# Kernel tuning notes

Measured on AMD Instinct MI355X. Metric: run time of the kernel, lower is better.

The kernel has to match this reference:

```python
import jax, jax.numpy as jnp
import numpy as np
from jax import lax

C = 64
KD = 16  # in_channels // k_factor
KS = 3
DN = ('NCHW', 'OIHW', 'NCHW')


def setup_inputs() -> dict:
    key = jax.random.key(0)
    ks = jax.random.split(key, 9)
    B, H, W = 4, 128, 128
    s = 0.05
    return {
        'x': jax.random.normal(ks[0], (B, C, H, W), jnp.float32),
        'y': jax.random.normal(ks[1], (B, C, H, W), jnp.float32),
        'z': jax.random.normal(ks[2], (B, C, H, W), jnp.float32),
        'Wq': jax.random.normal(ks[3], (C, 1, KS, KS), jnp.float32) * s,   # depthwise
        'bq': jax.random.normal(ks[4], (C,), jnp.float32) * s,
        'Wk': jax.random.normal(ks[5], (KD, C, KS, KS), jnp.float32) * s,
        'bk': jax.random.normal(ks[6], (KD,), jnp.float32) * s,
        'wv': jax.random.normal(ks[7], (KD,), jnp.float32) * s,           # 1x1 conv 1->KD
        'bv': jax.random.normal(ks[8], (KD,), jnp.float32) * s,
    }


def reference(x, y, z, Wq, bq, Wk, bk, wv, bv):
    # Q: depthwise 3x3 conv + ReLU on y -> [B,C,H,W]
    q = jax.nn.relu(
        lax.conv_general_dilated(y, Wq, (1, 1), 'SAME',
                                 dimension_numbers=DN, feature_group_count=C)
        + bq[None, :, None, None])
    # K: 3x3 conv C->KD + ReLU on x -> [B,KD,H,W], shared across the C channel axis
    k = jax.nn.relu(
        lax.conv_general_dilated(x, Wk, (1, 1), 'SAME', dimension_numbers=DN)
        + bk[None, :, None, None])
    # V: 1x1 conv 1->KD + ReLU applied per input channel of z -> [B,C,KD,H,W]
    v = jax.nn.relu(z[:, :, None] * wv[None, None, :, None, None]
                    + bv[None, None, :, None, None])
    # Degenerate SDPA: head_dim=1 so scale=1; softmax over the KD 'sequence' axis.
    scores = q[:, :, None] * k[:, None]              # [B,C,KD,H,W]
    attn = jax.nn.softmax(scores, axis=2)
    return jnp.sum(attn * v, axis=2)                 # [B,C,H,W]
```

## Files before the change

kernel.cpp:

```cpp
#include <hip/hip_runtime.h>

#define HH 128
#define WW 128
#define CC 64
#define KD 16
#define HW (HH * WW)
#define HWB (HW * 4)
#define TOTBYTES (4u * CC * HW * 4u)
#define OOB_SENT 0x40000000

using int32x4_t = __attribute__((ext_vector_type(4))) int;
using floatx4   = __attribute__((ext_vector_type(4))) float;

__device__ floatx4 llvm_amdgcn_raw_buffer_load_v4f32(int32x4_t srsrc, int voffset,
                                                     int soffset, int aux)
    __asm("llvm.amdgcn.raw.buffer.load.v4f32");
__device__ float llvm_amdgcn_raw_buffer_load_f32(int32x4_t srsrc, int voffset,
                                                 int soffset, int aux)
    __asm("llvm.amdgcn.raw.buffer.load.f32");

__device__ inline int32x4_t make_srd(const void* p, unsigned bytes) {
    const unsigned long long a = (unsigned long long)p;
    int32x4_t r;
    r.x = (int)(a & 0xffffffffull);
    r.y = (int)(a >> 32);
    r.z = (int)bytes;
    r.w = 0x00020000;
    return r;
}

#if __has_builtin(__builtin_amdgcn_exp2f)
#define FAST_EXP2(x) __builtin_amdgcn_exp2f(x)
#define KLOG2E 1.44269504088896340736f
#else
#define FAST_EXP2(x) __expf(x)
#define KLOG2E 1.0f
#endif

__global__ __launch_bounds__(512, 8) void gatev_fused(
    const float* __restrict__ x, const float* __restrict__ y,
    const float* __restrict__ z,
    const float* __restrict__ Wq, const float* __restrict__ bq,
    const float* __restrict__ Wk, const float* __restrict__ bk,
    const float* __restrict__ wv, const float* __restrict__ bv,
    float* __restrict__ out)
{
    __shared__ float part[8 * KD * 64];

    const int tid  = threadIdx.x;
    const int g    = __builtin_amdgcn_readfirstlane(tid >> 6);
    const int lane = tid & 63;
    const int px   = lane & 15, py = lane >> 4;
    const int b    = blockIdx.z;
    const int h    = blockIdx.y * 4 + py;
    const int w    = blockIdx.x * 16 + px;
    const int pix  = h * WW + w;

    const int32x4_t rx = make_srd(x, TOTBYTES);
    const int32x4_t ry = make_srd(y, TOTBYTES);
    const int32x4_t rz = make_srd(z, TOTBYTES);

    const int colb = (w > 0 ? w - 1 : 0) * 4;
    int rowB[3];
#pragma unroll
    for (int r = 0; r < 3; ++r) {
        const int rr = h - 1 + r;
        rowB[r] = (rr >= 0 && rr < HH) ? rr * WW * 4 + colb : OOB_SENT;
    }
    const float mL = (w > 0) ? 1.f : 0.f;
    const float mR = (w < WW - 1) ? 1.f : 0.f;
    const bool  w0 = (w == 0);

    const int base = b * CC * HWB;
    const int c0   = __builtin_amdgcn_readfirstlane(g * 8);

    auto taps9 = [&](const int32x4_t& srd, int so, float (&tp)[9]) {
#pragma unroll
        for (int r = 0; r < 3; ++r) {
            const floatx4 f = llvm_amdgcn_raw_buffer_load_v4f32(srd, rowB[r], so, 0);
            tp[r * 3 + 0] = f.x * mL;
            tp[r * 3 + 1] = w0 ? f.x : f.y;
            tp[r * 3 + 2] = (w0 ? f.y : f.z) * mR;
        }
    };

    float acc[KD];
#pragma unroll
    for (int d = 0; d < KD; ++d) acc[d] = 0.f;

    for (int ci = 0; ci < 8; ++ci) {
        const int c = c0 + ci;
        float tp[9];
        taps9(rx, base + c * HWB, tp);
        const float* wp = Wk + c * 9;
#pragma unroll
        for (int d = 0; d < KD; ++d)
#pragma unroll
            for (int t = 0; t < 9; ++t)
                acc[d] = fmaf(wp[d * (CC * 9) + t], tp[t], acc[d]);
    }
#pragma unroll
    for (int d = 0; d < KD; ++d)
        part[g * (KD * 64) + d * 64 + lane] = acc[d];
    __syncthreads();

#pragma unroll
    for (int rep = 0; rep < 2; ++rep) {
        const int idx = tid + rep * 512;
        float s = part[idx];
#pragma unroll
        for (int gg = 1; gg < 8; ++gg) s += part[gg * (KD * 64) + idx];
        const int d = idx >> 6;
        part[idx] = fmaxf(s + bk[d], 0.f) * KLOG2E;
    }
    __syncthreads();

    float q[8], zv[8];
#pragma unroll 2
    for (int ci = 0; ci < 8; ++ci) {
        const int c  = c0 + ci;
        const int so = base + c * HWB;
        float tp[9];
        taps9(ry, so, tp);
        const float* wq = Wq + c * 9;
        float a = 0.f;
#pragma unroll
        for (int t = 0; t < 9; ++t) a = fmaf(wq[t], tp[t], a);
        q[ci]  = fmaxf(a + bq[c], 0.f);
        zv[ci] = llvm_amdgcn_raw_buffer_load_f32(rz, pix * 4, so, 0);
    }

    float num[8], den[8];
#pragma unroll
    for (int ci = 0; ci < 8; ++ci) { num[ci] = 0.f; den[ci] = 0.f; }

#pragma unroll
    for (int d = 0; d < KD; ++d) {
        const float kl  = part[d * 64 + lane];
        const float wvd = wv[d];
        const float bvd = bv[d];
#pragma unroll
        for (int ci = 0; ci < 8; ++ci) {
            const float e = FAST_EXP2(q[ci] * kl);
            const float v = fmaxf(zv[ci] * wvd + bvd, 0.f);
            num[ci] = fmaf(e, v, num[ci]);
            den[ci] += e;
        }
    }

    float* ob = out + (size_t)b * CC * HW;
#pragma unroll
    for (int ci = 0; ci < 8; ++ci)
        ob[(c0 + ci) * HW + pix] = __fdividef(num[ci], den[ci]);
}

extern "C" void kernel_launch(void* const* d_in, const int* in_sizes, int n_in,
                              void* d_out, int out_size, void* d_ws, size_t ws_size,
                              hipStream_t stream) {
    const float* x  = (const float*)d_in[0];
    const float* y  = (const float*)d_in[1];
    const float* z  = (const float*)d_in[2];
    const float* Wq = (const float*)d_in[3];
    const float* bq = (const float*)d_in[4];
    const float* Wk = (const float*)d_in[5];
    const float* bk = (const float*)d_in[6];
    const float* wv = (const float*)d_in[7];
    const float* bv = (const float*)d_in[8];
    float* out = (float*)d_out;

    dim3 grid(WW / 16, HH / 4, 4);
    dim3 block(512);
    hipLaunchKernelGGL(gatev_fused, grid, block, 0, stream,
                       x, y, z, Wq, bq, Wk, bk, wv, bv, out);
}
```

Before: 51.18 us.

## Compute K convolution with FP16 MFMA from an LDS-staged halo tile

Replaces the per-thread scalar FP32 3x3 C->KD convolution with an implicit GEMM on MFMA 16x16x32 f16 instructions. The x halo tile (6x18x64) and the Wk weights are converted to fp16 and staged in swizzled LDS, and eight waves each cover one output row and one half of the channels. The partial-sum reduction shrinks from 8 groups to 2. This cuts the FP32 FMA work of the K conv, at the cost of fp16 rounding of the inputs and weights (a precision risk), a larger LDS footprint that may lower occupancy, and an extra barrier.

Measured after the change: 84.38 us. 64.9% more time.

```diff
diff --git a/kernel.cpp b/kernel.cpp
--- a/kernel.cpp
+++ b/kernel.cpp
@@ -9,8 +9,9 @@
 #define TOTBYTES (4u * CC * HW * 4u)
 #define OOB_SENT 0x40000000
 
-using int32x4_t = __attribute__((ext_vector_type(4))) int;
-using floatx4   = __attribute__((ext_vector_type(4))) float;
+typedef __attribute__((ext_vector_type(4))) int   int32x4_t;
+typedef __attribute__((ext_vector_type(4))) float floatx4;
+typedef _Float16 f16x8 __attribute__((ext_vector_type(8)));
 
 __device__ floatx4 llvm_amdgcn_raw_buffer_load_v4f32(int32x4_t srsrc, int voffset,
                                                      int soffset, int aux)
@@ -45,88 +46,131 @@
     const float* __restrict__ wv, const float* __restrict__ bv,
     float* __restrict__ out)
 {
-    __shared__ float part[8 * KD * 64];
+    __shared__ __align__(16) unsigned char smem[40960];
+    unsigned short* xt   = (unsigned short*)smem;
+    unsigned short* wkl  = (unsigned short*)(smem + 14336);
+    float*          part = (float*)(smem + 32768);
 
     const int tid  = threadIdx.x;
     const int g    = __builtin_amdgcn_readfirstlane(tid >> 6);
     const int lane = tid & 63;
     const int px   = lane & 15, py = lane >> 4;
     const int b    = blockIdx.z;
-    const int h    = blockIdx.y * 4 + py;
-    const int w    = blockIdx.x * 16 + px;
+    const int h0   = blockIdx.y * 4;
+    const int w0   = blockIdx.x * 16;
+    const int h    = h0 + py;
+    const int w    = w0 + px;
     const int pix  = h * WW + w;
 
     const int32x4_t rx = make_srd(x, TOTBYTES);
     const int32x4_t ry = make_srd(y, TOTBYTES);
     const int32x4_t rz = make_srd(z, TOTBYTES);
 
+    const int base = b * CC * HWB;
+
+#pragma unroll
+    for (int rep = 0; rep < 7; ++rep) {
+        const int idx2 = tid + rep * 512;
+        const int e0   = idx2 * 2;
+        const int c    = e0 & 63;
+        const int pos  = e0 >> 6;
+        if (pos < 108) {
+            const int row = pos / 18, col = pos - row * 18;
+            const int ir = h0 - 1 + row, ic = w0 - 1 + col;
+            const int voff = ((unsigned)ir < (unsigned)HH && (unsigned)ic < (unsigned)WW)
+                             ? (ir * WW + ic) * 4 : OOB_SENT;
+            const float a = llvm_amdgcn_raw_buffer_load_f32(rx, voff, base + c * HWB, 0);
+            const float bv2 = llvm_amdgcn_raw_buffer_load_f32(rx, voff, base + (c + 1) * HWB, 0);
+            const unsigned short ua = __builtin_bit_cast(unsigned short, (_Float16)a);
+            const unsigned short ub = __builtin_bit_cast(unsigned short, (_Float16)bv2);
+            const int gsw  = ((c >> 3) ^ (col & 7));
+            const int addr = pos * 64 + gsw * 8 + (c & 7);
+            *(unsigned*)(xt + addr) = (unsigned)ua | ((unsigned)ub << 16);
+        }
+    }
+
+#pragma unroll
+    for (int rep = 0; rep < 9; ++rep) {
+        const int idx2 = tid + rep * 512;
+        const int e0   = idx2 * 2;
+        const int c    = e0 & 63;
+        const int d    = (e0 >> 6) & 15;
+        const int t    = e0 >> 10;
+        const float a   = Wk[(d * CC + c) * 9 + t];
+        const float b2  = Wk[(d * CC + c + 1) * 9 + t];
+        const unsigned short ua = __builtin_bit_cast(unsigned short, (_Float16)a);
+        const unsigned short ub = __builtin_bit_cast(unsigned short, (_Float16)b2);
+        const int gsw  = ((c >> 3) ^ (d & 7));
+        const int addr = (t * 16 + d) * 64 + gsw * 8 + (c & 7);
+        *(unsigned*)(wkl + addr) = (unsigned)ua | ((unsigned)ub << 16);
+    }
+    __syncthreads();
+
+    {
+        const int r  = g & 3;
+        const int cv = g >> 2;
+        const int m  = lane & 15;
+        const int q  = lane >> 4;
+
+        floatx4 acc = {0.f, 0.f, 0.f, 0.f};
+#pragma unroll
+        for (int t = 0; t < 9; ++t) {
+            const int trow = t / 3, tcol = t % 3;
+            const int ga = (cv * 4 + q) ^ (m & 7);
+            const f16x8 af = *(const f16x8*)(wkl + ((t * 16 + m) * 64 + ga * 8));
+            const int col = m + tcol;
+            const int pos = (r + trow) * 18 + col;
+            const int gb  = (cv * 4 + q) ^ (col & 7);
+            const f16x8 bf = *(const f16x8*)(xt + (pos * 64 + gb * 8));
+            acc = __builtin_amdgcn_mfma_f32_16x16x32_f16(af, bf, acc, 0, 0, 0);
+        }
+        const int pbase = (cv * 16 + q * 4) * 64 + r * 16 + m;
+#pragma unroll
+        for (int i = 0; i < 4; ++i)
+            part[pbase + i * 64] = acc[i];
+    }
+    __syncthreads();
+
+#pragma unroll
+    for (int rep = 0; rep < 2; ++rep) {
+        const int idx = tid + rep * 512;
+        const int d   = idx >> 6;
+        const float s = part[idx] + part[1024 + idx];
+        part[idx] = fmaxf(s + bk[d], 0.f) * KLOG2E;
+    }
+    __syncthreads();
+
     const int colb = (w > 0 ? w - 1 : 0) * 4;
     int rowB[3];
 #pragma unroll
-    for (int r = 0; r < 3; ++r) {
-        const int rr = h - 1 + r;
-        rowB[r] = (rr >= 0 && rr < HH) ? rr * WW * 4 + colb : OOB_SENT;
+    for (int r3 = 0; r3 < 3; ++r3) {
+        const int rr = h - 1 + r3;
+        rowB[r3] = (rr >= 0 && rr < HH) ? rr * WW * 4 + colb : OOB_SENT;
     }
     const float mL = (w > 0) ? 1.f : 0.f;
     const float mR = (w < WW - 1) ? 1.f : 0.f;
-    const bool  w0 = (w == 0);
-
-    const int base = b * CC * HWB;
-    const int c0   = __builtin_amdgcn_readfirstlane(g * 8);
-
-    auto taps9 = [&](const int32x4_t& srd, int so, float (&tp)[9]) {
-#pragma unroll
-        for (int r = 0; r < 3; ++r) {
-            const floatx4 f = llvm_amdgcn_raw_buffer_load_v4f32(srd, rowB[r], so, 0);
-            tp[r * 3 + 0] = f.x * mL;
-            tp[r * 3 + 1] = w0 ? f.x : f.y;
-            tp[r * 3 + 2] = (w0 ? f.y : f.z) * mR;
-        }
-    };
-
-    float acc[KD];
-#pragma unroll
-    for (int d = 0; d < KD; ++d) acc[d] = 0.f;
-
-    for (int ci = 0; ci < 8; ++ci) {
-        const int c = c0 + ci;
-        float tp[9];
-        taps9(rx, base + c * HWB, tp);
-        const float* wp = Wk + c * 9;
-#pragma unroll
-        for (int d = 0; d < KD; ++d)
-#pragma unroll
-            for (int t = 0; t < 9; ++t)
-                acc[d] = fmaf(wp[d * (CC * 9) + t], tp[t], acc[d]);
-    }
-#pragma unroll
-    for (int d = 0; d < KD; ++d)
-        part[g * (KD * 64) + d * 64 + lane] = acc[d];
-    __syncthreads();
-
-#pragma unroll
-    for (int rep = 0; rep < 2; ++rep) {
-        const int idx = tid + rep * 512;
-        float s = part[idx];
-#pragma unroll
-        for (int gg = 1; gg < 8; ++gg) s += part[gg * (KD * 64) + idx];
-        const int d = idx >> 6;
-        part[idx] = fmaxf(s + bk[d], 0.f) * KLOG2E;
-    }
-    __syncthreads();
-
-    float q[8], zv[8];
+    const bool  w0e = (w == 0);
+
+    const int c0 = __builtin_amdgcn_readfirstlane(g * 8);
+
+    float qv[8], zv[8];
 #pragma unroll 2
     for (int ci = 0; ci < 8; ++ci) {
         const int c  = c0 + ci;
         const int so = base + c * HWB;
-        float tp[9];
-        taps9(ry, so, tp);
         const float* wq = Wq + c * 9;
         float a = 0.f;
 #pragma unroll
-        for (int t = 0; t < 9; ++t) a = fmaf(wq[t], tp[t], a);
-        q[ci]  = fmaxf(a + bq[c], 0.f);
+        for (int r3 = 0; r3 < 3; ++r3) {
+            const floatx4 f = llvm_amdgcn_raw_buffer_load_v4f32(ry, rowB[r3], so, 0);
+            const float tL = f.x * mL;
+            const float tC = w0e ? f.x : f.y;
+            const float tR = (w0e ? f.y : f.z) * mR;
+            a = fmaf(wq[r3 * 3 + 0], tL, a);
+            a = fmaf(wq[r3 * 3 + 1], tC, a);
+            a = fmaf(wq[r3 * 3 + 2], tR, a);
+        }
+        qv[ci] = fmaxf(a + bq[c], 0.f);
         zv[ci] = llvm_amdgcn_raw_buffer_load_f32(rz, pix * 4, so, 0);
     }
 
@@ -141,7 +185,7 @@
         const float bvd = bv[d];
 #pragma unroll
         for (int ci = 0; ci < 8; ++ci) {
-            const float e = FAST_EXP2(q[ci] * kl);
+            const float e = FAST_EXP2(qv[ci] * kl);
             const float v = fmaxf(zv[ci] * wvd + bvd, 0.f);
             num[ci] = fmaf(e, v, num[ci]);
             den[ci] += e;
```

## Stage Wk in LDS and double-buffer x tap loads in K conv

Applied to the files above, without the earlier changes.

Each block first copies the full Wk weight tensor into shared memory, transposed so that each wave's channel slice is contiguous and can be read with vector LDS loads. Before, those weights came from scalar/global loads. The K-convolution loop is fully unrolled with two register buffers, so the next channel's x rows are fetched while the current channel is computed. The shared buffer grows to 36 KB and is reused for the partial-sum reduction. The costs are an extra barrier, the per-block weight copy, higher register pressure, and a shared-memory footprint that may reduce occupancy.

Measured after the change: 48.51 us. 1.06x faster.

```diff
diff --git a/kernel.cpp b/kernel.cpp
--- a/kernel.cpp
+++ b/kernel.cpp
@@ -9,8 +9,8 @@
 #define TOTBYTES (4u * CC * HW * 4u)
 #define OOB_SENT 0x40000000
 
-using int32x4_t = __attribute__((ext_vector_type(4))) int;
-using floatx4   = __attribute__((ext_vector_type(4))) float;
+typedef __attribute__((ext_vector_type(4))) int   int32x4_t;
+typedef __attribute__((ext_vector_type(4))) float floatx4;
 
 __device__ floatx4 llvm_amdgcn_raw_buffer_load_v4f32(int32x4_t srsrc, int voffset,
                                                      int soffset, int aux)
@@ -45,7 +45,7 @@
     const float* __restrict__ wv, const float* __restrict__ bv,
     float* __restrict__ out)
 {
-    __shared__ float part[8 * KD * 64];
+    __shared__ float wk_lds[9216];
 
     const int tid  = threadIdx.x;
     const int g    = __builtin_amdgcn_readfirstlane(tid >> 6);
@@ -69,64 +69,96 @@
     }
     const float mL = (w > 0) ? 1.f : 0.f;
     const float mR = (w < WW - 1) ? 1.f : 0.f;
-    const bool  w0 = (w == 0);
+    const bool  w0e = (w == 0);
 
     const int base = b * CC * HWB;
     const int c0   = __builtin_amdgcn_readfirstlane(g * 8);
 
-    auto taps9 = [&](const int32x4_t& srd, int so, float (&tp)[9]) {
+#pragma unroll
+    for (int p = 0; p < 18; ++p) {
+        const int s   = p * 512 + tid;
+        const int d   = s / 576;
+        const int rem = s - d * 576;
+        const int c   = rem / 9;
+        const int t   = rem - c * 9;
+        wk_lds[(c >> 3) * 1152 + (c & 7) * 144 + d * 9 + t] = Wk[s];
+    }
+    __syncthreads();
+
+    float acc[KD];
+#pragma unroll
+    for (int d = 0; d < KD; ++d) acc[d] = 0.f;
+
+    auto load3 = [&](floatx4 (&f)[3], int so) {
+#pragma unroll
+        for (int r = 0; r < 3; ++r)
+            f[r] = llvm_amdgcn_raw_buffer_load_v4f32(rx, rowB[r], so, 0);
+    };
+    auto compute = [&](const floatx4 (&f)[3], int wb) {
+        float tp[9];
 #pragma unroll
         for (int r = 0; r < 3; ++r) {
-            const floatx4 f = llvm_amdgcn_raw_buffer_load_v4f32(srd, rowB[r], so, 0);
-            tp[r * 3 + 0] = f.x * mL;
-            tp[r * 3 + 1] = w0 ? f.x : f.y;
-            tp[r * 3 + 2] = (w0 ? f.y : f.z) * mR;
+            tp[r * 3 + 0] = f[r].x * mL;
+            tp[r * 3 + 1] = w0e ? f[r].x : f[r].y;
+            tp[r * 3 + 2] = (w0e ? f[r].y : f[r].z) * mR;
+        }
+#pragma unroll
+        for (int i = 0; i < 36; ++i) {
+            const floatx4 wf = *(const floatx4*)&wk_lds[wb + i * 4];
+#pragma unroll
+            for (int j = 0; j < 4; ++j) {
+                const int flat = i * 4 + j;
+                acc[flat / 9] = fmaf(wf[j], tp[flat % 9], acc[flat / 9]);
+            }
         }
     };
 
-    float acc[KD];
-#pragma unroll
-    for (int d = 0; d < KD; ++d) acc[d] = 0.f;
-
-    for (int ci = 0; ci < 8; ++ci) {
-        const int c = c0 + ci;
-        float tp[9];
-        taps9(rx, base + c * HWB, tp);
-        const float* wp = Wk + c * 9;
-#pragma unroll
-        for (int d = 0; d < KD; ++d)
-#pragma unroll
-            for (int t = 0; t < 9; ++t)
-                acc[d] = fmaf(wp[d * (CC * 9) + t], tp[t], acc[d]);
-    }
+    const int wbase = g * 1152;
+    floatx4 f0[3], f1[3];
+    load3(f0, base + c0 * HWB);
+#pragma unroll
+    for (int cp = 0; cp < 4; ++cp) {
+        load3(f1, base + (c0 + 2 * cp + 1) * HWB);
+        compute(f0, wbase + (2 * cp) * 144);
+        load3(f0, base + (c0 + 2 * cp + 2) * HWB);
+        compute(f1, wbase + (2 * cp + 1) * 144);
+    }
+    __syncthreads();
+
 #pragma unroll
     for (int d = 0; d < KD; ++d)
-        part[g * (KD * 64) + d * 64 + lane] = acc[d];
+        wk_lds[g * (KD * 64) + d * 64 + lane] = acc[d];
     __syncthreads();
 
 #pragma unroll
     for (int rep = 0; rep < 2; ++rep) {
         const int idx = tid + rep * 512;
-        float s = part[idx];
-#pragma unroll
-        for (int gg = 1; gg < 8; ++gg) s += part[gg * (KD * 64) + idx];
+        float s = wk_lds[idx];
+#pragma unroll
+        for (int gg = 1; gg < 8; ++gg) s += wk_lds[gg * (KD * 64) + idx];
         const int d = idx >> 6;
-        part[idx] = fmaxf(s + bk[d], 0.f) * KLOG2E;
-    }
-    __syncthreads();
-
-    float q[8], zv[8];
+        wk_lds[idx] = fmaxf(s + bk[d], 0.f) * KLOG2E;
+    }
+    __syncthreads();
+
+    float qv[8], zv[8];
 #pragma unroll 2
     for (int ci = 0; ci < 8; ++ci) {
         const int c  = c0 + ci;
         const int so = base + c * HWB;
-        float tp[9];
-        taps9(ry, so, tp);
         const float* wq = Wq + c * 9;
         float a = 0.f;
 #pragma unroll
-        for (int t = 0; t < 9; ++t) a = fmaf(wq[t], tp[t], a);
-        q[ci]  = fmaxf(a + bq[c], 0.f);
+        for (int r = 0; r < 3; ++r) {
+            const floatx4 f = llvm_amdgcn_raw_buffer_load_v4f32(ry, rowB[r], so, 0);
+            const float tL = f.x * mL;
+            const float tC = w0e ? f.x : f.y;
+            const float tR = (w0e ? f.y : f.z) * mR;
+            a = fmaf(wq[r * 3 + 0], tL, a);
+            a = fmaf(wq[r * 3 + 1], tC, a);
+            a = fmaf(wq[r * 3 + 2], tR, a);
+        }
+        qv[ci] = fmaxf(a + bq[c], 0.f);
         zv[ci] = llvm_amdgcn_raw_buffer_load_f32(rz, pix * 4, so, 0);
     }
 
@@ -136,12 +168,12 @@
 
 #pragma unroll
     for (int d = 0; d < KD; ++d) {
-        const float kl  = part[d * 64 + lane];
+        const float kl  = wk_lds[d * 64 + lane];
         const float wvd = wv[d];
         const float bvd = bv[d];
 #pragma unroll
         for (int ci = 0; ci < 8; ++ci) {
-            const float e = FAST_EXP2(q[ci] * kl);
+            const float e = FAST_EXP2(qv[ci] * kl);
             const float v = fmaxf(zv[ci] * wvd + bvd, 0.f);
             num[ci] = fmaf(e, v, num[ci]);
             den[ci] += e;
```
